# Optimization experiments

Measured on AMD Instinct MI355X. Metric: run time of the kernel, lower is better.

## Reference

```python
import jax, jax.numpy as jnp
import numpy as np

D_EMB, N_HEADS = 1024, 16
D_K = D_EMB // N_HEADS

def setup_inputs() -> dict:
    key = jax.random.key(0)
    ks = jax.random.split(key, 5)
    scale = 0.02
    return {
        "n": jax.random.normal(ks[0], (2, 2048, D_EMB), dtype=jnp.float32),
        "W_q": jax.random.normal(ks[1], (D_EMB, D_EMB), dtype=jnp.float32) * scale,
        "W_k": jax.random.normal(ks[2], (D_EMB, D_EMB), dtype=jnp.float32) * scale,
        "W_v": jax.random.normal(ks[3], (D_EMB, D_EMB), dtype=jnp.float32) * scale,
        "W_o": jax.random.normal(ks[4], (D_EMB, D_EMB), dtype=jnp.float32) * scale,
    }

def reference(n, W_q, W_k, W_v, W_o):
    B, S, _ = n.shape
    # torch Linear(bias=False): y = x @ W.T, W is [out, in]
    def proj(x, W):
        y = jnp.einsum('bsd,ed->bse', x, W)
        return y.reshape(B, S, N_HEADS, D_K).transpose(0, 2, 1, 3)  # [B,H,S,Dk]
    Q, K, V = proj(n, W_q), proj(n, W_k), proj(n, W_v)
    A = jnp.einsum('bhqd,bhkd->bhqk', Q, K) * (D_K ** -0.5)
    A = jnp.clip(A, -5.0, 5.0)
    A = jax.nn.softmax(A, axis=-1)
    ctx = jnp.einsum('bhqk,bhkd->bhqd', A, V)  # [B,H,S,Dk]
    ctx = ctx.transpose(0, 2, 1, 3).reshape(B, S, D_EMB)
    return jnp.einsum('bsd,ed->bse', ctx, W_o)
```

## Files before the change

kernel.cpp:

```cpp
#include <hip/hip_runtime.h>
#include <hip/hip_bf16.h>
#include <stdint.h>

typedef __attribute__((ext_vector_type(4))) float floatx4;
typedef __attribute__((ext_vector_type(8))) short shortx8;
typedef __attribute__((ext_vector_type(4))) unsigned short ushortx4;
typedef __attribute__((ext_vector_type(8))) unsigned short ushortx8;

#define MFMA16(a, b, c) __builtin_amdgcn_mfma_f32_16x16x32_bf16((a), (b), (c), 0, 0, 0)

__device__ inline unsigned short f2bf(float f) {
    union { float f; uint32_t u; } v; v.f = f;
    uint32_t u = v.u;
    return (unsigned short)((u + 0x7FFFu + ((u >> 16) & 1u)) >> 16);
}

__device__ inline uint32_t pkbf(float a, float b) {
    return ((uint32_t)f2bf(b) << 16) | f2bf(a);
}

__device__ inline void gl2lds16(const void* g, void* l) {
    __builtin_amdgcn_global_load_lds(
        (const __attribute__((address_space(1))) void*)(uintptr_t)g,
        (__attribute__((address_space(3))) void*)(uintptr_t)l, 16, 0, 0);
}

__global__ void convert_all(const float* __restrict__ n, const float* __restrict__ wq,
                            const float* __restrict__ wk, const float* __restrict__ wv,
                            const float* __restrict__ wo,
                            unsigned short* __restrict__ nb, unsigned short* __restrict__ wqb,
                            unsigned short* __restrict__ wkb, unsigned short* __restrict__ wvb,
                            unsigned short* __restrict__ wob) {
    int i = blockIdx.x * 256 + threadIdx.x;
    const float* src; unsigned short* dst; int off;
    if (i < 1048576) { src = n; dst = nb; off = i; }
    else {
        int j = i - 1048576; int r = j >> 18; int o = j & 262143;
        src = (r == 0) ? wq : (r == 1) ? wk : (r == 2) ? wv : wo;
        dst = (r == 0) ? wqb : (r == 1) ? wkb : (r == 2) ? wvb : wob;
        off = o;
    }
    floatx4 f = ((const floatx4*)src)[off];
    ushortx4 h;
    h.x = f2bf(f.x); h.y = f2bf(f.y); h.z = f2bf(f.z); h.w = f2bf(f.w);
    ((ushortx4*)dst)[off] = h;
}

__device__ inline void gemm_tile_128(const unsigned short* __restrict__ A,
                                     const unsigned short* __restrict__ B,
                                     unsigned short* sA, unsigned short* sB,
                                     floatx4 acc[4][4]) {
    const int tid = threadIdx.x, w = tid >> 6, l = tid & 63;
    const int c = l & 15, quad = l >> 4;
    const int wm = (w >> 1) * 64, wn = (w & 1) * 64;
    for (int kt = 0; kt < 16; ++kt) {
        #pragma unroll
        for (int r = 0; r < 4; ++r) {
            int row = r * 32 + w * 8 + (l >> 3);
            int cb  = (l & 7) ^ (row & 7);
            gl2lds16(A + row * 1024 + kt * 64 + cb * 8, (char*)sA + r * 4096 + w * 1024 + l * 16);
            gl2lds16(B + row * 1024 + kt * 64 + cb * 8, (char*)sB + r * 4096 + w * 1024 + l * 16);
        }
        __syncthreads();
        #pragma unroll
        for (int ks = 0; ks < 2; ++ks) {
            shortx8 af[4], bfr[4];
            #pragma unroll
            for (int i2 = 0; i2 < 4; ++i2) {
                int ra = wm + i2 * 16 + c;
                af[i2] = *(const shortx8*)((const char*)sA + ra * 128 + (((ks * 4 + quad) ^ (ra & 7)) * 16));
                int rb = wn + i2 * 16 + c;
                bfr[i2] = *(const shortx8*)((const char*)sB + rb * 128 + (((ks * 4 + quad) ^ (rb & 7)) * 16));
            }
            #pragma unroll
            for (int i2 = 0; i2 < 4; ++i2)
                #pragma unroll
                for (int j2 = 0; j2 < 4; ++j2)
                    acc[i2][j2] = MFMA16(af[i2], bfr[j2], acc[i2][j2]);
        }
        __syncthreads();
    }
}

__global__ void gemm_qkv(const unsigned short* __restrict__ nb,
                         const unsigned short* __restrict__ wqb,
                         const unsigned short* __restrict__ wkb,
                         const unsigned short* __restrict__ wvb,
                         unsigned short* __restrict__ Qb, unsigned short* __restrict__ Kb,
                         unsigned short* __restrict__ VTg) {
    __shared__ unsigned short sAB[2 * 128 * 64];
    unsigned short* sA = sAB;
    unsigned short* sB = sAB + 128 * 64;
    const int mt = blockIdx.x, nt = blockIdx.y;
    const int region = nt >> 3, nl0 = (nt & 7) * 128;
    const unsigned short* W = (region == 0) ? wqb : (region == 1) ? wkb : wvb;
    floatx4 acc[4][4] = {};
    gemm_tile_128(nb + mt * 128 * 1024, W + nl0 * 1024, sA, sB, acc);
    const int tid = threadIdx.x, w = tid >> 6, l = tid & 63, c = l & 15, quad = l >> 4;
    const int wm = (w >> 1) * 64, wn = (w & 1) * 64;
    if (region < 2) {
        unsigned short* O = (region == 0) ? Qb : Kb;
        #pragma unroll
        for (int i2 = 0; i2 < 4; ++i2)
            #pragma unroll
            for (int j2 = 0; j2 < 4; ++j2)
                #pragma unroll
                for (int r = 0; r < 4; ++r) {
                    int row = wm + i2 * 16 + quad * 4 + r, col = wn + j2 * 16 + c;
                    sAB[row * 128 + col] = f2bf(acc[i2][j2][r]);
                }
        __syncthreads();
        #pragma unroll
        for (int t = 0; t < 8; ++t) {
            int off = t * 4096 + tid * 16;
            int row = off >> 8, colb = off & 255;
            *(ushortx8*)((char*)(O + (mt * 128 + row) * 1024 + nl0) + colb) =
                *(const ushortx8*)((const char*)sAB + off);
        }
    } else {
        #pragma unroll
        for (int i2 = 0; i2 < 4; ++i2)
            #pragma unroll
            for (int j2 = 0; j2 < 4; ++j2) {
                int m = mt * 128 + wm + i2 * 16 + quad * 4;
                int e = nl0 + wn + j2 * 16 + c;
                int h = e >> 6, d = e & 63;
                int t = m >> 6, k = m & 63;
                int j = k >> 4;
                int blk = (j >> 1) * 4 + quad;
                int phys = blk ^ (d & 7);
                char* p = (char*)VTg + h * 524288 + t * 8192 + d * 128 + phys * 16 + (j & 1) * 8;
                ushortx4 v;
                v.x = f2bf(acc[i2][j2][0]); v.y = f2bf(acc[i2][j2][1]);
                v.z = f2bf(acc[i2][j2][2]); v.w = f2bf(acc[i2][j2][3]);
                *(ushortx4*)p = v;
            }
    }
}

__global__ void gemm_out(const unsigned short* __restrict__ ctx,
                         const unsigned short* __restrict__ wob,
                         float* __restrict__ out) {
    __shared__ unsigned short sAB[2 * 128 * 64];
    unsigned short* sA = sAB;
    unsigned short* sB = sAB + 128 * 64;
    const int mt = blockIdx.x, nt = blockIdx.y;
    floatx4 acc[4][4] = {};
    gemm_tile_128(ctx + mt * 128 * 1024, wob + nt * 128 * 1024, sA, sB, acc);
    const int tid = threadIdx.x, w = tid >> 6, l = tid & 63, c = l & 15, quad = l >> 4;
    const int wn = (w & 1) * 64;
    float* sC = (float*)sAB;
    #pragma unroll
    for (int h = 0; h < 2; ++h) {
        if ((w >> 1) == h) {
            #pragma unroll
            for (int i2 = 0; i2 < 4; ++i2)
                #pragma unroll
                for (int j2 = 0; j2 < 4; ++j2)
                    #pragma unroll
                    for (int r = 0; r < 4; ++r) {
                        int row = i2 * 16 + quad * 4 + r, col = wn + j2 * 16 + c;
                        sC[row * 128 + col] = acc[i2][j2][r];
                    }
        }
        __syncthreads();
        #pragma unroll
        for (int t = 0; t < 8; ++t) {
            int off = t * 4096 + tid * 16;
            int row = off >> 9, colb = off & 511;
            *(floatx4*)((char*)(out + (mt * 128 + h * 64 + row) * 1024 + nt * 128) + colb) =
                *(const floatx4*)((const char*)sC + off);
        }
        __syncthreads();
    }
}

__global__ void attn(const unsigned short* __restrict__ Qb, const unsigned short* __restrict__ Kb,
                     const unsigned short* __restrict__ VTg, unsigned short* __restrict__ ctx) {
    __shared__ unsigned short sQ[128 * 64];
    __shared__ unsigned short sK[64 * 64];
    __shared__ unsigned short sV[64 * 64];
    const int qt = blockIdx.x, h = blockIdx.y, b = blockIdx.z;
    const int tid = threadIdx.x, w = tid >> 6, l = tid & 63, c = l & 15, quad = l >> 4;
    const int tok0 = b * 2048 + qt * 128;
    #pragma unroll
    for (int r = 0; r < 4; ++r) {
        int row = r * 32 + w * 8 + (l >> 3);
        int cb  = (l & 7) ^ (row & 7);
        gl2lds16(Qb + (tok0 + row) * 1024 + h * 64 + cb * 8, (char*)sQ + r * 4096 + w * 1024 + l * 16);
    }
    floatx4 cacc[4][2] = {};
    float lacc[2] = {0.f, 0.f};
    for (int kt = 0; kt < 32; ++kt) {
        #pragma unroll
        for (int r = 0; r < 2; ++r) {
            int row = r * 32 + w * 8 + (l >> 3);
            int cb  = (l & 7) ^ (row & 7);
            gl2lds16(Kb + (b * 2048 + kt * 64 + row) * 1024 + h * 64 + cb * 8,
                     (char*)sK + r * 4096 + w * 1024 + l * 16);
            gl2lds16((const char*)VTg + h * 524288 + (b * 32 + kt) * 8192 + w * 2048 + r * 1024 + l * 16,
                     (char*)sV + w * 2048 + r * 1024 + l * 16);
        }
        __syncthreads();
        floatx4 s[2][4] = {};
        #pragma unroll
        for (int ks = 0; ks < 2; ++ks) {
            shortx8 ak[4], qf[2];
            #pragma unroll
            for (int j = 0; j < 4; ++j) {
                int rk = j * 16 + c;
                ak[j] = *(const shortx8*)((const char*)sK + rk * 128 + (((ks * 4 + quad) ^ (rk & 7)) * 16));
            }
            #pragma unroll
            for (int qb = 0; qb < 2; ++qb) {
                int rq = w * 32 + qb * 16 + c;
                qf[qb] = *(const shortx8*)((const char*)sQ + rq * 128 + (((ks * 4 + quad) ^ (rq & 7)) * 16));
            }
            #pragma unroll
            for (int j = 0; j < 4; ++j)
                #pragma unroll
                for (int qb = 0; qb < 2; ++qb)
                    s[qb][j] = MFMA16(ak[j], qf[qb], s[qb][j]);
        }
        #pragma unroll
        for (int qb = 0; qb < 2; ++qb) {
            float rs = 0.f;
            #pragma unroll
            for (int j = 0; j < 4; ++j)
                #pragma unroll
                for (int r = 0; r < 4; ++r) {
                    float v = s[qb][j][r] * 0.125f;
                    v = fminf(fmaxf(v, -5.f), 5.f);
                    v = __expf(v);
                    s[qb][j][r] = v;
                    rs += v;
                }
            rs += __shfl_xor(rs, 16);
            rs += __shfl_xor(rs, 32);
            lacc[qb] += rs;
        }
        #pragma unroll
        for (int chunk = 0; chunk < 2; ++chunk) {
            shortx8 av[4];
            #pragma unroll
            for (int di = 0; di < 4; ++di) {
                int rv = di * 16 + c;
                av[di] = *(const shortx8*)((const char*)sV + rv * 128 + (((chunk * 4 + quad) ^ (rv & 7)) * 16));
            }
            shortx8 p[2];
            #pragma unroll
            for (int qb = 0; qb < 2; ++qb) {
                union { shortx8 v; uint32_t u[4]; } pk;
                pk.u[0] = pkbf(s[qb][2 * chunk][0], s[qb][2 * chunk][1]);
                pk.u[1] = pkbf(s[qb][2 * chunk][2], s[qb][2 * chunk][3]);
                pk.u[2] = pkbf(s[qb][2 * chunk + 1][0], s[qb][2 * chunk + 1][1]);
                pk.u[3] = pkbf(s[qb][2 * chunk + 1][2], s[qb][2 * chunk + 1][3]);
                p[qb] = pk.v;
            }
            #pragma unroll
            for (int di = 0; di < 4; ++di)
                #pragma unroll
                for (int qb = 0; qb < 2; ++qb)
                    cacc[di][qb] = MFMA16(av[di], p[qb], cacc[di][qb]);
        }
        __syncthreads();
    }
    #pragma unroll
    for (int qb = 0; qb < 2; ++qb) {
        float inv = 1.0f / lacc[qb];
        int row = tok0 + w * 32 + qb * 16 + c;
        #pragma unroll
        for (int di = 0; di < 4; ++di) {
            ushortx4 v;
            v.x = f2bf(cacc[di][qb][0] * inv);
            v.y = f2bf(cacc[di][qb][1] * inv);
            v.z = f2bf(cacc[di][qb][2] * inv);
            v.w = f2bf(cacc[di][qb][3] * inv);
            *(ushortx4*)(ctx + row * 1024 + h * 64 + di * 16 + quad * 4) = v;
        }
    }
}

extern "C" void kernel_launch(void* const* d_in, const int* in_sizes, int n_in,
                              void* d_out, int out_size, void* d_ws, size_t ws_size,
                              hipStream_t stream) {
    const float* n  = (const float*)d_in[0];
    const float* wq = (const float*)d_in[1];
    const float* wk = (const float*)d_in[2];
    const float* wv = (const float*)d_in[3];
    const float* wo = (const float*)d_in[4];
    float* out = (float*)d_out;
    char* ws = (char*)d_ws;
    unsigned short* nb  = (unsigned short*)(ws);
    unsigned short* wqb = (unsigned short*)(ws + 8388608);
    unsigned short* wkb = (unsigned short*)(ws + 10485760);
    unsigned short* wvb = (unsigned short*)(ws + 12582912);
    unsigned short* wob = (unsigned short*)(ws + 14680064);
    unsigned short* Qb  = (unsigned short*)(ws + 16777216);
    unsigned short* Kb  = (unsigned short*)(ws + 25165824);
    unsigned short* VTg = (unsigned short*)(ws + 33554432);
    unsigned short* ctx = (unsigned short*)(ws + 41943040);

    convert_all<<<dim3(8192), dim3(256), 0, stream>>>(n, wq, wk, wv, wo, nb, wqb, wkb, wvb, wob);
    gemm_qkv<<<dim3(32, 24), dim3(256), 0, stream>>>(nb, wqb, wkb, wvb, Qb, Kb, VTg);
    attn<<<dim3(16, 16, 2), dim3(256), 0, stream>>>(Qb, Kb, VTg, ctx);
    gemm_out<<<dim3(32, 8), dim3(256), 0, stream>>>(ctx, wob, out);
}
```

Baseline: 197.0 us.

## Double-buffer attention K/V, stage V^T via LDS, retile output GEMM, use hardware bf16/exp2

Attention now double-buffers K and V tiles in LDS so the next tile's global-to-LDS load overlaps current compute, hoists Q fragments out of the loop, and folds the scale and clip into an exp2 formulation. The QKV GEMM writes V^T through an LDS staging image so global stores are coalesced 16-byte rows. The output GEMM uses 128x64 tiles (twice the blocks) for better CU occupancy, and bf16 packing uses the hardware cvt_pk instruction where available. The extra LDS for double buffering may reduce occupancy, and exp2 with a folded constant slightly changes rounding.

Result: faster. 190.6 us (-3.2%).

```diff
diff --git a/kernel.cpp b/kernel.cpp
--- a/kernel.cpp
+++ b/kernel.cpp
@@ -6,6 +6,7 @@
 typedef __attribute__((ext_vector_type(8))) short shortx8;
 typedef __attribute__((ext_vector_type(4))) unsigned short ushortx4;
 typedef __attribute__((ext_vector_type(8))) unsigned short ushortx8;
+typedef __attribute__((ext_vector_type(2))) uint32_t uintx2;
 
 #define MFMA16(a, b, c) __builtin_amdgcn_mfma_f32_16x16x32_bf16((a), (b), (c), 0, 0, 0)
 
@@ -15,9 +16,22 @@
     return (unsigned short)((u + 0x7FFFu + ((u >> 16) & 1u)) >> 16);
 }
 
+#if defined(__has_builtin) && __has_builtin(__builtin_amdgcn_cvt_pk_bf16_f32)
+__device__ inline uint32_t pkbf(float a, float b) {
+    auto r = __builtin_amdgcn_cvt_pk_bf16_f32(a, b);
+    union { decltype(r) v; uint32_t u; } x; x.v = r; return x.u;
+}
+#else
 __device__ inline uint32_t pkbf(float a, float b) {
     return ((uint32_t)f2bf(b) << 16) | f2bf(a);
 }
+#endif
+
+#if defined(__has_builtin) && __has_builtin(__builtin_amdgcn_exp2f)
+#define EXP2F(x) __builtin_amdgcn_exp2f(x)
+#else
+#define EXP2F(x) __expf((x) * 0.69314718056f)
+#endif
 
 __device__ inline void gl2lds16(const void* g, void* l) {
     __builtin_amdgcn_global_load_lds(
@@ -41,9 +55,9 @@
         off = o;
     }
     floatx4 f = ((const floatx4*)src)[off];
-    ushortx4 h;
-    h.x = f2bf(f.x); h.y = f2bf(f.y); h.z = f2bf(f.z); h.w = f2bf(f.w);
-    ((ushortx4*)dst)[off] = h;
+    uintx2 u;
+    u.x = pkbf(f.x, f.y); u.y = pkbf(f.z, f.w);
+    ((uintx2*)dst)[off] = u;
 }
 
 __device__ inline void gemm_tile_128(const unsigned short* __restrict__ A,
@@ -118,109 +132,166 @@
                 *(const ushortx8*)((const char*)sAB + off);
         }
     } else {
+        const int hh = w & 1, tt = w >> 1;
+        char* img = (char*)sAB + (hh * 2 + tt) * 8192;
         #pragma unroll
         for (int i2 = 0; i2 < 4; ++i2)
             #pragma unroll
             for (int j2 = 0; j2 < 4; ++j2) {
-                int m = mt * 128 + wm + i2 * 16 + quad * 4;
-                int e = nl0 + wn + j2 * 16 + c;
-                int h = e >> 6, d = e & 63;
-                int t = m >> 6, k = m & 63;
-                int j = k >> 4;
-                int blk = (j >> 1) * 4 + quad;
+                int d = j2 * 16 + c;
+                int blk = (i2 >> 1) * 4 + quad;
                 int phys = blk ^ (d & 7);
-                char* p = (char*)VTg + h * 524288 + t * 8192 + d * 128 + phys * 16 + (j & 1) * 8;
-                ushortx4 v;
-                v.x = f2bf(acc[i2][j2][0]); v.y = f2bf(acc[i2][j2][1]);
-                v.z = f2bf(acc[i2][j2][2]); v.w = f2bf(acc[i2][j2][3]);
-                *(ushortx4*)p = v;
-            }
-    }
-}
-
-__global__ void gemm_out(const unsigned short* __restrict__ ctx,
+                uintx2 v;
+                v.x = pkbf(acc[i2][j2][0], acc[i2][j2][1]);
+                v.y = pkbf(acc[i2][j2][2], acc[i2][j2][3]);
+                *(uintx2*)(img + d * 128 + phys * 16 + (i2 & 1) * 8) = v;
+            }
+        __syncthreads();
+        const int h0 = (nt & 7) * 2, t0 = mt * 2;
+        #pragma unroll
+        for (int g = 0; g < 8; ++g) {
+            int off = g * 4096 + tid * 16;
+            int hsel = off >> 14, within = off & 16383;
+            *(ushortx8*)((char*)VTg + (h0 + hsel) * 524288 + t0 * 8192 + within) =
+                *(const ushortx8*)((const char*)sAB + off);
+        }
+    }
+}
+
+__global__ void __launch_bounds__(256) gemm_out(const unsigned short* __restrict__ ctx,
                          const unsigned short* __restrict__ wob,
                          float* __restrict__ out) {
-    __shared__ unsigned short sAB[2 * 128 * 64];
-    unsigned short* sA = sAB;
-    unsigned short* sB = sAB + 128 * 64;
+    __shared__ unsigned short sA[128 * 64];
+    __shared__ unsigned short sB[64 * 64];
+    __shared__ float sC[64 * 64];
     const int mt = blockIdx.x, nt = blockIdx.y;
-    floatx4 acc[4][4] = {};
-    gemm_tile_128(ctx + mt * 128 * 1024, wob + nt * 128 * 1024, sA, sB, acc);
+    const unsigned short* A = ctx + mt * 128 * 1024;
+    const unsigned short* B = wob + nt * 64 * 1024;
     const int tid = threadIdx.x, w = tid >> 6, l = tid & 63, c = l & 15, quad = l >> 4;
-    const int wn = (w & 1) * 64;
-    float* sC = (float*)sAB;
-    #pragma unroll
-    for (int h = 0; h < 2; ++h) {
-        if ((w >> 1) == h) {
-            #pragma unroll
-            for (int i2 = 0; i2 < 4; ++i2)
+    const int srow = w * 8 + (l >> 3), scb = l & 7;
+    floatx4 acc[2][4] = {};
+    for (int kt = 0; kt < 16; ++kt) {
+        #pragma unroll
+        for (int r = 0; r < 4; ++r) {
+            int row = r * 32 + srow, cb = scb ^ (row & 7);
+            gl2lds16(A + row * 1024 + kt * 64 + cb * 8, (char*)sA + r * 4096 + w * 1024 + l * 16);
+        }
+        #pragma unroll
+        for (int r = 0; r < 2; ++r) {
+            int row = r * 32 + srow, cb = scb ^ (row & 7);
+            gl2lds16(B + row * 1024 + kt * 64 + cb * 8, (char*)sB + r * 4096 + w * 1024 + l * 16);
+        }
+        __syncthreads();
+        #pragma unroll
+        for (int ks = 0; ks < 2; ++ks) {
+            shortx8 af[2], bf2[4];
+            #pragma unroll
+            for (int i2 = 0; i2 < 2; ++i2) {
+                int ra = w * 32 + i2 * 16 + c;
+                af[i2] = *(const shortx8*)((const char*)sA + ra * 128 + (((ks * 4 + quad) ^ (ra & 7)) * 16));
+            }
+            #pragma unroll
+            for (int j2 = 0; j2 < 4; ++j2) {
+                int rb = j2 * 16 + c;
+                bf2[j2] = *(const shortx8*)((const char*)sB + rb * 128 + (((ks * 4 + quad) ^ (rb & 7)) * 16));
+            }
+            #pragma unroll
+            for (int i2 = 0; i2 < 2; ++i2)
+                #pragma unroll
+                for (int j2 = 0; j2 < 4; ++j2)
+                    acc[i2][j2] = MFMA16(af[i2], bf2[j2], acc[i2][j2]);
+        }
+        __syncthreads();
+    }
+    #pragma unroll
+    for (int half = 0; half < 2; ++half) {
+        if ((w >> 1) == half) {
+            #pragma unroll
+            for (int i2 = 0; i2 < 2; ++i2)
                 #pragma unroll
                 for (int j2 = 0; j2 < 4; ++j2)
                     #pragma unroll
                     for (int r = 0; r < 4; ++r) {
-                        int row = i2 * 16 + quad * 4 + r, col = wn + j2 * 16 + c;
-                        sC[row * 128 + col] = acc[i2][j2][r];
+                        int row = (w & 1) * 32 + i2 * 16 + quad * 4 + r, col = j2 * 16 + c;
+                        sC[row * 64 + col] = acc[i2][j2][r];
                     }
         }
         __syncthreads();
         #pragma unroll
-        for (int t = 0; t < 8; ++t) {
+        for (int t = 0; t < 4; ++t) {
             int off = t * 4096 + tid * 16;
-            int row = off >> 9, colb = off & 511;
-            *(floatx4*)((char*)(out + (mt * 128 + h * 64 + row) * 1024 + nt * 128) + colb) =
+            int row = off >> 8, colb = off & 255;
+            *(floatx4*)((char*)(out + (mt * 128 + half * 64 + row) * 1024 + nt * 64) + colb) =
                 *(const floatx4*)((const char*)sC + off);
         }
         __syncthreads();
     }
 }
 
-__global__ void attn(const unsigned short* __restrict__ Qb, const unsigned short* __restrict__ Kb,
+__global__ void __launch_bounds__(256) attn(const unsigned short* __restrict__ Qb,
+                     const unsigned short* __restrict__ Kb,
                      const unsigned short* __restrict__ VTg, unsigned short* __restrict__ ctx) {
     __shared__ unsigned short sQ[128 * 64];
-    __shared__ unsigned short sK[64 * 64];
-    __shared__ unsigned short sV[64 * 64];
+    __shared__ unsigned short sK[2][64 * 64];
+    __shared__ unsigned short sV[2][64 * 64];
     const int qt = blockIdx.x, h = blockIdx.y, b = blockIdx.z;
     const int tid = threadIdx.x, w = tid >> 6, l = tid & 63, c = l & 15, quad = l >> 4;
     const int tok0 = b * 2048 + qt * 128;
+    const int srow = w * 8 + (l >> 3), scb = l & 7;
     #pragma unroll
     for (int r = 0; r < 4; ++r) {
-        int row = r * 32 + w * 8 + (l >> 3);
-        int cb  = (l & 7) ^ (row & 7);
+        int row = r * 32 + srow, cb = scb ^ (row & 7);
         gl2lds16(Qb + (tok0 + row) * 1024 + h * 64 + cb * 8, (char*)sQ + r * 4096 + w * 1024 + l * 16);
     }
+    const unsigned short* Kbase = Kb + b * 2048 * 1024 + h * 64;
+    const char* Vbase = (const char*)VTg + h * 524288 + (size_t)b * 32 * 8192;
+    #pragma unroll
+    for (int r = 0; r < 2; ++r) {
+        int row = r * 32 + srow, cb = scb ^ (row & 7);
+        gl2lds16(Kbase + row * 1024 + cb * 8, (char*)sK[0] + r * 4096 + w * 1024 + l * 16);
+        gl2lds16(Vbase + r * 4096 + w * 1024 + l * 16, (char*)sV[0] + r * 4096 + w * 1024 + l * 16);
+    }
+    __syncthreads();
+    shortx8 qf[2][2];
+    #pragma unroll
+    for (int ks = 0; ks < 2; ++ks)
+        #pragma unroll
+        for (int qb = 0; qb < 2; ++qb) {
+            int rq = w * 32 + qb * 16 + c;
+            qf[ks][qb] = *(const shortx8*)((const char*)sQ + rq * 128 + (((ks * 4 + quad) ^ (rq & 7)) * 16));
+        }
     floatx4 cacc[4][2] = {};
     float lacc[2] = {0.f, 0.f};
+    const float SC = 0.18033688f;
+    const float CLIP = 7.2134752f;
     for (int kt = 0; kt < 32; ++kt) {
-        #pragma unroll
-        for (int r = 0; r < 2; ++r) {
-            int row = r * 32 + w * 8 + (l >> 3);
-            int cb  = (l & 7) ^ (row & 7);
-            gl2lds16(Kb + (b * 2048 + kt * 64 + row) * 1024 + h * 64 + cb * 8,
-                     (char*)sK + r * 4096 + w * 1024 + l * 16);
-            gl2lds16((const char*)VTg + h * 524288 + (b * 32 + kt) * 8192 + w * 2048 + r * 1024 + l * 16,
-                     (char*)sV + w * 2048 + r * 1024 + l * 16);
-        }
-        __syncthreads();
+        const int cur = kt & 1;
+        if (kt < 31) {
+            #pragma unroll
+            for (int r = 0; r < 2; ++r) {
+                int row = r * 32 + srow, cb = scb ^ (row & 7);
+                gl2lds16(Kbase + ((kt + 1) * 64 + row) * 1024 + cb * 8,
+                         (char*)sK[cur ^ 1] + r * 4096 + w * 1024 + l * 16);
+                gl2lds16(Vbase + (kt + 1) * 8192 + r * 4096 + w * 1024 + l * 16,
+                         (char*)sV[cur ^ 1] + r * 4096 + w * 1024 + l * 16);
+            }
+        }
+        const unsigned short* sKc = sK[cur];
+        const unsigned short* sVc = sV[cur];
         floatx4 s[2][4] = {};
         #pragma unroll
         for (int ks = 0; ks < 2; ++ks) {
-            shortx8 ak[4], qf[2];
+            shortx8 ak[4];
             #pragma unroll
             for (int j = 0; j < 4; ++j) {
                 int rk = j * 16 + c;
-                ak[j] = *(const shortx8*)((const char*)sK + rk * 128 + (((ks * 4 + quad) ^ (rk & 7)) * 16));
-            }
-            #pragma unroll
-            for (int qb = 0; qb < 2; ++qb) {
-                int rq = w * 32 + qb * 16 + c;
-                qf[qb] = *(const shortx8*)((const char*)sQ + rq * 128 + (((ks * 4 + quad) ^ (rq & 7)) * 16));
+                ak[j] = *(const shortx8*)((const char*)sKc + rk * 128 + (((ks * 4 + quad) ^ (rk & 7)) * 16));
             }
             #pragma unroll
             for (int j = 0; j < 4; ++j)
                 #pragma unroll
                 for (int qb = 0; qb < 2; ++qb)
-                    s[qb][j] = MFMA16(ak[j], qf[qb], s[qb][j]);
+                    s[qb][j] = MFMA16(ak[j], qf[ks][qb], s[qb][j]);
         }
         #pragma unroll
         for (int qb = 0; qb < 2; ++qb) {
@@ -229,9 +300,9 @@
             for (int j = 0; j < 4; ++j)
                 #pragma unroll
                 for (int r = 0; r < 4; ++r) {
-                    float v = s[qb][j][r] * 0.125f;
-                    v = fminf(fmaxf(v, -5.f), 5.f);
-                    v = __expf(v);
+                    float v = s[qb][j][r] * SC;
+                    v = fminf(fmaxf(v, -CLIP), CLIP);
+                    v = EXP2F(v);
                     s[qb][j][r] = v;
                     rs += v;
                 }
@@ -245,7 +316,7 @@
             #pragma unroll
             for (int di = 0; di < 4; ++di) {
                 int rv = di * 16 + c;
-                av[di] = *(const shortx8*)((const char*)sV + rv * 128 + (((chunk * 4 + quad) ^ (rv & 7)) * 16));
+                av[di] = *(const shortx8*)((const char*)sVc + rv * 128 + (((chunk * 4 + quad) ^ (rv & 7)) * 16));
             }
             shortx8 p[2];
             #pragma unroll
@@ -263,7 +334,7 @@
                 for (int qb = 0; qb < 2; ++qb)
                     cacc[di][qb] = MFMA16(av[di], p[qb], cacc[di][qb]);
         }
-        __syncthreads();
+        if (kt < 31) __syncthreads();
     }
     #pragma unroll
     for (int qb = 0; qb < 2; ++qb) {
@@ -271,12 +342,10 @@
         int row = tok0 + w * 32 + qb * 16 + c;
         #pragma unroll
         for (int di = 0; di < 4; ++di) {
-            ushortx4 v;
-            v.x = f2bf(cacc[di][qb][0] * inv);
-            v.y = f2bf(cacc[di][qb][1] * inv);
-            v.z = f2bf(cacc[di][qb][2] * inv);
-            v.w = f2bf(cacc[di][qb][3] * inv);
-            *(ushortx4*)(ctx + row * 1024 + h * 64 + di * 16 + quad * 4) = v;
+            uintx2 v;
+            v.x = pkbf(cacc[di][qb][0] * inv, cacc[di][qb][1] * inv);
+            v.y = pkbf(cacc[di][qb][2] * inv, cacc[di][qb][3] * inv);
+            *(uintx2*)(ctx + row * 1024 + h * 64 + di * 16 + quad * 4) = v;
         }
     }
 }
@@ -304,5 +373,5 @@
     convert_all<<<dim3(8192), dim3(256), 0, stream>>>(n, wq, wk, wv, wo, nb, wqb, wkb, wvb, wob);
     gemm_qkv<<<dim3(32, 24), dim3(256), 0, stream>>>(nb, wqb, wkb, wvb, Qb, Kb, VTg);
     attn<<<dim3(16, 16, 2), dim3(256), 0, stream>>>(Qb, Kb, VTg, ctx);
-    gemm_out<<<dim3(32, 8), dim3(256), 0, stream>>>(ctx, wob, out);
-}
+    gemm_out<<<dim3(32, 16), dim3(256), 0, stream>>>(ctx, wob, out);
+}
```
